# Kernel optimization log

Measured on AMD Instinct MI355X. Metric: run time of the kernel, lower is better.

## Reference

```python
import jax, jax.numpy as jnp
import numpy as np

EPS = 1e-6
TOPK = 5            # k = min(5, n_cluster)
SIGMA_HI = 1e4      # 10000 upper bound of binary search


def _pairwise_dist(z, mu, eps):
    # torch: sqrt(sum_d (z_id - mu_jd + eps)^2). Expanded algebraically to avoid the
    # (N, K, D) broadcast intermediate: (a-b+e)^2 = a^2 + b^2 + e^2 - 2ab + 2e(a-b).
    Dh = z.shape[1]
    z2 = jnp.sum(z * z, axis=1, keepdims=True)            # (N,1)
    m2 = jnp.sum(mu * mu, axis=1)[None, :]                # (1,K)
    cross = z @ mu.T                                      # (N,K)
    lin = 2.0 * eps * (jnp.sum(z, axis=1, keepdims=True) - jnp.sum(mu, axis=1)[None, :])
    d2 = z2 + m2 - 2.0 * cross + lin + Dh * (eps * eps)
    return jnp.sqrt(jnp.maximum(d2, 0.0))


def _calibrate_sigmas(rel_z, rel_u, rho_z, rho_u, k):
    # UMAP-style binary search. rel_z: (N,k) smallest dists per sample (ascending),
    # rel_u: (K,k) smallest dists per center. sigma values only ever flow from the
    # constant {0, SIGMA_HI} bounds, so this carries no gradient (matches torch).
    N = rel_z.shape[0]
    K = rel_u.shape[0]
    target = np.float32(np.log2(k) - 1.0)
    target1 = np.float32(np.log2(k))
    mid_z = jnp.concatenate([jnp.zeros((N, 1), jnp.float32), SIGMA_HI * jnp.ones((N, 1), jnp.float32)], axis=1)
    sigma_z = jnp.ones((N, 1), jnp.float32)
    mid_u = jnp.concatenate([jnp.zeros((K, 1), jnp.float32), SIGMA_HI * jnp.ones((K, 1), jnp.float32)], axis=1)
    sigma_u = jnp.ones((1, K), jnp.float32)
    rel_u_t = rel_u.T                                     # (k,K)

    def body(state, _):
        mid_u, sigma_u, mid_z, sigma_z = state
        current_u = jnp.sum(jnp.exp(-jax.nn.relu(rel_u_t - rho_u) / sigma_u), axis=0)   # (K,)
        idx_u = (current_u > target1).astype(jnp.int32)
        mid_u = mid_u.at[jnp.arange(K), idx_u].set(sigma_u[0])
        sigma_u = jnp.mean(mid_u, axis=1)[None, :]
        current_z = jnp.sum(jnp.exp(-jax.nn.relu(rel_z - rho_z) / sigma_z), axis=1)     # (N,)
        idx_z = (current_z > target).astype(jnp.int32)
        mid_z = mid_z.at[jnp.arange(N), idx_z].set(sigma_z[:, 0])
        sigma_z = jnp.mean(mid_z, axis=1)[:, None]
        return (mid_u, sigma_u, mid_z, sigma_z), None

    state, _ = jax.lax.scan(body, (mid_u, sigma_u, mid_z, sigma_z), None, length=k * 30)
    return state[3], state[1]  # sigma_z (N,1), sigma_u (1,K)


def compute_S(z, mu, epoch):
    sg = jax.lax.stop_gradient
    d_ = _pairwise_dist(z, mu, EPS)                       # (N,K)
    k = min(TOPK, mu.shape[0])
    rel_z = -jax.lax.top_k(-d_, k)[0]                     # (N,k) k smallest, ascending
    rel_u = -jax.lax.top_k(-d_.T, k)[0]                   # (K,k)
    rho_z = rel_z[:, :1]                                  # (N,1) nearest center per sample
    rho_u = rel_u[:, 0][None, :]                          # (1,K) nearest sample per center
    sigma_z, sigma_u = _calibrate_sigmas(sg(rel_z), sg(rel_u), sg(rho_z), sg(rho_u), k)
    rho_z = sg(rho_z)                                     # torch .detach()
    rho_u = sg(rho_u)
    W1 = jnp.exp(-jax.nn.relu(d_ - rho_z) / sigma_z)      # (N,K)
    W2 = jnp.exp(-jax.nn.relu(d_ - rho_u) / sigma_u)      # (N,K)
    S = W1 + W2 - W1 * W2
    S = S / jnp.sum(S, axis=1, keepdims=True)
    Dmat = (S * S) / jnp.sum(S, axis=0)                   # column-normalized sharpening
    Dmat = Dmat / jnp.sum(Dmat, axis=1, keepdims=True)
    return (W1, S, W1, Dmat)


def setup_inputs() -> dict:
    key = jax.random.key(0)
    kz, km = jax.random.split(key)
    z = jax.random.normal(kz, (65536, 256), dtype=jnp.float32)
    mu = jax.random.normal(km, (256, 256), dtype=jnp.float32)
    return {"z": z, "mu": mu, "epoch": 1}


def reference(z, mu, epoch):
    return compute_S(z, mu, epoch)
```

## Files before the change

### kernel.cpp

```cpp
#include <hip/hip_runtime.h>
#include <math.h>
#include <float.h>

#define KN 65536
#define KK 256
#define KD 256
#define KNK (65536LL * 256LL)
#define EPS_C 1e-6f
#define TARGET_Z 1.3219280948873622f
#define TARGET_U 2.3219280948873622f


__device__ __forceinline__ void ins5(float v, float& t0, float& t1, float& t2,
                                     float& t3, float& t4) {
    if (v < t4) {
        t4 = v; float tmp;
        if (t4 < t3) { tmp = t3; t3 = t4; t4 = tmp; }
        if (t3 < t2) { tmp = t2; t2 = t3; t3 = tmp; }
        if (t2 < t1) { tmp = t1; t1 = t2; t2 = tmp; }
        if (t1 < t0) { tmp = t0; t0 = t1; t1 = tmp; }
    }
}

__device__ __forceinline__ float bisect_sigma(float g1, float g2, float g3,
                                              float g4, float target) {
    float lo = 0.f, hi = 10000.f, sigma = 1.f;
    #pragma unroll 1
    for (int it = 0; it < 150; ++it) {
        float inv = 1.f / sigma;
        float s = 1.f + expf(-g1 * inv) + expf(-g2 * inv) +
                  expf(-g3 * inv) + expf(-g4 * inv);
        if (s > target) hi = sigma; else lo = sigma;
        sigma = 0.5f * (lo + hi);
    }
    return sigma;
}


__global__ __launch_bounds__(256) void row_stats(const float* __restrict__ x,
                                                 float* __restrict__ xs,
                                                 float* __restrict__ x2) {
    int wave = threadIdx.x >> 6, lane = threadIdx.x & 63;
    int row = blockIdx.x * 4 + wave;
    const float4* p = (const float4*)(x + (size_t)row * KD);
    float4 v = p[lane];
    float s = v.x + v.y + v.z + v.w;
    float q = v.x * v.x + v.y * v.y + v.z * v.z + v.w * v.w;
    #pragma unroll
    for (int off = 32; off > 0; off >>= 1) {
        s += __shfl_down(s, off, 64);
        q += __shfl_down(q, off, 64);
    }
    if (lane == 0) { xs[row] = s; x2[row] = q; }
}

__global__ __launch_bounds__(256) void dist_gemm(const float* __restrict__ z,
                                                 const float* __restrict__ mu,
                                                 const float* __restrict__ zs,
                                                 const float* __restrict__ z2,
                                                 const float* __restrict__ ms,
                                                 const float* __restrict__ m2,
                                                 float* __restrict__ dout) {
    __shared__ __align__(16) float As[16][132];
    __shared__ __align__(16) float Bs[16][132];
    int tid = threadIdx.x;
    int r0 = blockIdx.y * 128;
    int c0 = blockIdx.x * 128;
    int tx = tid & 15, ty = tid >> 4;
    float acc[8][8];
    #pragma unroll
    for (int i = 0; i < 8; ++i)
        #pragma unroll
        for (int j = 0; j < 8; ++j) acc[i][j] = 0.f;

    for (int kk = 0; kk < KD; kk += 16) {
        #pragma unroll
        for (int i = 0; i < 2; ++i) {
            int f = tid + 256 * i;
            int row = f >> 2, q = f & 3;
            float4 va = *(const float4*)(z + (size_t)(r0 + row) * KD + kk + 4 * q);
            As[4 * q + 0][row] = va.x; As[4 * q + 1][row] = va.y;
            As[4 * q + 2][row] = va.z; As[4 * q + 3][row] = va.w;
            float4 vb = *(const float4*)(mu + (size_t)(c0 + row) * KD + kk + 4 * q);
            Bs[4 * q + 0][row] = vb.x; Bs[4 * q + 1][row] = vb.y;
            Bs[4 * q + 2][row] = vb.z; Bs[4 * q + 3][row] = vb.w;
        }
        __syncthreads();
        #pragma unroll
        for (int k = 0; k < 16; ++k) {
            float4 a0 = *(const float4*)&As[k][ty * 8];
            float4 a1 = *(const float4*)&As[k][ty * 8 + 4];
            float4 b0 = *(const float4*)&Bs[k][tx * 8];
            float4 b1 = *(const float4*)&Bs[k][tx * 8 + 4];
            float a[8] = {a0.x, a0.y, a0.z, a0.w, a1.x, a1.y, a1.z, a1.w};
            float b[8] = {b0.x, b0.y, b0.z, b0.w, b1.x, b1.y, b1.z, b1.w};
            #pragma unroll
            for (int i = 0; i < 8; ++i)
                #pragma unroll
                for (int j = 0; j < 8; ++j) acc[i][j] += a[i] * b[j];
        }
        __syncthreads();
    }
    #pragma unroll
    for (int i = 0; i < 8; ++i) {
        int r = r0 + ty * 8 + i;
        float z2r = z2[r], zsr = zs[r];
        float out[8];
        #pragma unroll
        for (int j = 0; j < 8; ++j) {
            int c = c0 + tx * 8 + j;
            float d2 = z2r + m2[c] - 2.f * acc[i][j] +
                       2.f * EPS_C * (zsr - ms[c]) + (float)KD * EPS_C * EPS_C;
            out[j] = sqrtf(fmaxf(d2, 0.f));
        }
        float4* dst = (float4*)(dout + (size_t)r * KK + c0 + tx * 8);
        dst[0] = make_float4(out[0], out[1], out[2], out[3]);
        dst[1] = make_float4(out[4], out[5], out[6], out[7]);
    }
}

__global__ __launch_bounds__(256) void row_top5_sigma(const float* __restrict__ d,
                                                      float* __restrict__ rho_z,
                                                      float* __restrict__ isz) {
    int row = blockIdx.x * 256 + threadIdx.x;
    const float4* p = (const float4*)(d + (size_t)row * KK);
    float t0 = FLT_MAX, t1 = FLT_MAX, t2 = FLT_MAX, t3 = FLT_MAX, t4 = FLT_MAX;
    #pragma unroll 8
    for (int j = 0; j < KK / 4; ++j) {
        float4 v = p[j];
        ins5(v.x, t0, t1, t2, t3, t4); ins5(v.y, t0, t1, t2, t3, t4);
        ins5(v.z, t0, t1, t2, t3, t4); ins5(v.w, t0, t1, t2, t3, t4);
    }
    float sigma = bisect_sigma(t1 - t0, t2 - t0, t3 - t0, t4 - t0, TARGET_Z);
    rho_z[row] = t0;
    isz[row] = 1.f / sigma;
}

__global__ __launch_bounds__(256) void col_partial_top5(const float* __restrict__ d,
                                                        float* __restrict__ partials) {
    int b = blockIdx.x, t = threadIdx.x;
    size_t base = (size_t)b * 256 * KK + t;
    float t0 = FLT_MAX, t1 = FLT_MAX, t2 = FLT_MAX, t3 = FLT_MAX, t4 = FLT_MAX;
    #pragma unroll 8
    for (int r = 0; r < 256; ++r) ins5(d[base + (size_t)r * KK], t0, t1, t2, t3, t4);
    float* out = partials + ((size_t)t * 256 + b) * 5;
    out[0] = t0; out[1] = t1; out[2] = t2; out[3] = t3; out[4] = t4;
}

__global__ __launch_bounds__(64) void col_sigma(const float* __restrict__ partials,
                                                float* __restrict__ rho_u,
                                                float* __restrict__ isu) {
    int c = blockIdx.x * 64 + threadIdx.x;
    const float4* p = (const float4*)(partials + (size_t)c * 1280);
    float t0 = FLT_MAX, t1 = FLT_MAX, t2 = FLT_MAX, t3 = FLT_MAX, t4 = FLT_MAX;
    #pragma unroll 4
    for (int i = 0; i < 320; ++i) {
        float4 v = p[i];
        ins5(v.x, t0, t1, t2, t3, t4); ins5(v.y, t0, t1, t2, t3, t4);
        ins5(v.z, t0, t1, t2, t3, t4); ins5(v.w, t0, t1, t2, t3, t4);
    }
    float sigma = bisect_sigma(t1 - t0, t2 - t0, t3 - t0, t4 - t0, TARGET_U);
    rho_u[c] = t0;
    isu[c] = 1.f / sigma;
}

__global__ __launch_bounds__(256) void rowsum_su(const float* __restrict__ d,
                                                 const float* __restrict__ rho_z,
                                                 const float* __restrict__ isz,
                                                 const float* __restrict__ rho_u,
                                                 const float* __restrict__ isu,
                                                 float* __restrict__ irowsum) {
    int row = blockIdx.x * 256 + threadIdx.x;
    float rz = rho_z[row], sz = isz[row];
    const float4* p = (const float4*)(d + (size_t)row * KK);
    const float4* RU = (const float4*)rho_u;
    const float4* IU = (const float4*)isu;
    float sum = 0.f;
    #pragma unroll 4
    for (int j = 0; j < KK / 4; ++j) {
        float4 v = p[j], ru = RU[j], iu = IU[j];
        float w1, w2;
        w1 = expf(-fmaxf(v.x - rz, 0.f) * sz); w2 = expf(-fmaxf(v.x - ru.x, 0.f) * iu.x);
        sum += w1 + w2 - w1 * w2;
        w1 = expf(-fmaxf(v.y - rz, 0.f) * sz); w2 = expf(-fmaxf(v.y - ru.y, 0.f) * iu.y);
        sum += w1 + w2 - w1 * w2;
        w1 = expf(-fmaxf(v.z - rz, 0.f) * sz); w2 = expf(-fmaxf(v.z - ru.z, 0.f) * iu.z);
        sum += w1 + w2 - w1 * w2;
        w1 = expf(-fmaxf(v.w - rz, 0.f) * sz); w2 = expf(-fmaxf(v.w - ru.w, 0.f) * iu.w);
        sum += w1 + w2 - w1 * w2;
    }
    irowsum[row] = 1.f / sum;
}

__global__ __launch_bounds__(256) void w1_s_pass(const float* __restrict__ d,
                                                 const float* __restrict__ rho_z,
                                                 const float* __restrict__ isz,
                                                 const float* __restrict__ rho_u,
                                                 const float* __restrict__ isu,
                                                 const float* __restrict__ irowsum,
                                                 float* __restrict__ out0,
                                                 float* __restrict__ out1,
                                                 float* __restrict__ out2,
                                                 float* __restrict__ colsum) {
    int t = threadIdx.x;
    int r0 = blockIdx.x * 64;
    float ru = rho_u[t], iu = isu[t];
    float csum = 0.f;
    for (int r = 0; r < 64; ++r) {
        int row = r0 + r;
        size_t idx = (size_t)row * KK + t;
        float dv = d[idx];
        float rz = rho_z[row], sz = isz[row], ir = irowsum[row];
        float w1 = expf(-fmaxf(dv - rz, 0.f) * sz);
        float w2 = expf(-fmaxf(dv - ru, 0.f) * iu);
        float su = w1 + w2 - w1 * w2;
        float s = su * ir;
        out0[idx] = w1;
        out2[idx] = w1;
        out1[idx] = s;
        csum += s;
    }
    atomicAdd(&colsum[t], csum);
}

__global__ __launch_bounds__(256) void invert256(const float* __restrict__ colsum,
                                                 float* __restrict__ icol) {
    int t = threadIdx.x;
    icol[t] = 1.f / colsum[t];
}

__global__ __launch_bounds__(256) void rowsum_d(const float* __restrict__ S,
                                                const float* __restrict__ icol,
                                                float* __restrict__ irowD) {
    int row = blockIdx.x * 256 + threadIdx.x;
    const float4* p = (const float4*)(S + (size_t)row * KK);
    const float4* IC = (const float4*)icol;
    float sum = 0.f;
    #pragma unroll 4
    for (int j = 0; j < KK / 4; ++j) {
        float4 v = p[j], ic = IC[j];
        sum += v.x * v.x * ic.x + v.y * v.y * ic.y +
               v.z * v.z * ic.z + v.w * v.w * ic.w;
    }
    irowD[row] = 1.f / sum;
}

__global__ __launch_bounds__(256) void dmat_pass(const float* __restrict__ S,
                                                 const float* __restrict__ icol,
                                                 const float* __restrict__ irowD,
                                                 float* __restrict__ out3) {
    int t = threadIdx.x;
    int r0 = blockIdx.x * 64;
    float ic = icol[t];
    for (int r = 0; r < 64; ++r) {
        int row = r0 + r;
        size_t idx = (size_t)row * KK + t;
        float s = S[idx];
        out3[idx] = s * s * ic * irowD[row];
    }
}


extern "C" void kernel_launch(void* const* d_in, const int* in_sizes, int n_in,
                              void* d_out, int out_size, void* d_ws, size_t ws_size,
                              hipStream_t stream) {
    const float* z  = (const float*)d_in[0];
    const float* mu = (const float*)d_in[1];

    float* out = (float*)d_out;
    float* out0 = out;
    float* out1 = out + KNK;
    float* out2 = out + 2 * KNK;
    float* out3 = out + 3 * KNK;

    float* w = (float*)d_ws;
    float* zs       = w;
    float* z2       = w + KN;
    float* rho_z    = w + 2 * (size_t)KN;
    float* isz      = w + 3 * (size_t)KN;
    float* irowsum  = w + 4 * (size_t)KN;
    float* irowD    = w + 5 * (size_t)KN;
    float* ms       = w + 6 * (size_t)KN;
    float* m2       = ms + KK;
    float* rho_u    = m2 + KK;
    float* isu      = rho_u + KK;
    float* colsum   = isu + KK;
    float* icol     = colsum + KK;
    float* partials = icol + KK + 256;

    float* dmat = out3;

    hipMemsetAsync(colsum, 0, KK * sizeof(float), stream);

    row_stats<<<KN / 4, 256, 0, stream>>>(z, zs, z2);
    row_stats<<<KK / 4, 256, 0, stream>>>(mu, ms, m2);

    dist_gemm<<<dim3(KK / 128, KN / 128), 256, 0, stream>>>(z, mu, zs, z2, ms, m2, dmat);

    row_top5_sigma<<<KN / 256, 256, 0, stream>>>(dmat, rho_z, isz);

    col_partial_top5<<<KN / 256, 256, 0, stream>>>(dmat, partials);
    col_sigma<<<KK / 64, 64, 0, stream>>>(partials, rho_u, isu);

    rowsum_su<<<KN / 256, 256, 0, stream>>>(dmat, rho_z, isz, rho_u, isu, irowsum);

    w1_s_pass<<<KN / 64, 256, 0, stream>>>(dmat, rho_z, isz, rho_u, isu, irowsum,
                                           out0, out1, out2, colsum);

    invert256<<<1, 256, 0, stream>>>(colsum, icol);

    rowsum_d<<<KN / 256, 256, 0, stream>>>(out1, icol, irowD);

    dmat_pass<<<KN / 64, 256, 0, stream>>>(out1, icol, irowD, out3);
}
```

Baseline: 752.5 us.

## Fuse row top-5 and sigma into GEMM epilogue, fuse row-sum passes, coalesce column reductions

The distance GEMM now computes full 64x256 row tiles, so each block can extract the per-row top-5 with wave shuffles and run the sigma bisection in its epilogue. This removes the separate row top-5 kernel and its re-read of the distance matrix. The separate row-sum kernels for S and Dmat are folded into the element-wise passes by reducing across the 32 lanes that share a row. The column top-5 uses coalesced float4 loads plus a shared-memory merge, col_sigma uses one block per column with a shuffle merge, and bisection uses fast __expf. Trade-offs: more LDS use and register pressure in the GEMM, and slightly different exp precision.

```diff
diff --git a/kernel.cpp b/kernel.cpp
--- a/kernel.cpp
+++ b/kernel.cpp
@@ -9,6 +9,9 @@
 #define EPS_C 1e-6f
 #define TARGET_Z 1.3219280948873622f
 #define TARGET_U 2.3219280948873622f
+
+#define AS_LD 68
+#define BS_LD 260
 
 
 __device__ __forceinline__ void ins5(float v, float& t0, float& t1, float& t2,
@@ -28,8 +31,8 @@
     #pragma unroll 1
     for (int it = 0; it < 150; ++it) {
         float inv = 1.f / sigma;
-        float s = 1.f + expf(-g1 * inv) + expf(-g2 * inv) +
-                  expf(-g3 * inv) + expf(-g4 * inv);
+        float s = 1.f + __expf(-g1 * inv) + __expf(-g2 * inv) +
+                  __expf(-g3 * inv) + __expf(-g4 * inv);
         if (s > target) hi = sigma; else lo = sigma;
         sigma = 0.5f * (lo + hi);
     }
@@ -54,44 +57,51 @@
     if (lane == 0) { xs[row] = s; x2[row] = q; }
 }
 
-__global__ __launch_bounds__(256) void dist_gemm(const float* __restrict__ z,
-                                                 const float* __restrict__ mu,
-                                                 const float* __restrict__ zs,
-                                                 const float* __restrict__ z2,
-                                                 const float* __restrict__ ms,
-                                                 const float* __restrict__ m2,
-                                                 float* __restrict__ dout) {
-    __shared__ __align__(16) float As[16][132];
-    __shared__ __align__(16) float Bs[16][132];
+__global__ __launch_bounds__(256, 2) void dist_fused(
+    const float* __restrict__ z, const float* __restrict__ mu,
+    const float* __restrict__ zs, const float* __restrict__ z2,
+    const float* __restrict__ ms, const float* __restrict__ m2,
+    float* __restrict__ dout, float* __restrict__ rho_z,
+    float* __restrict__ isz) {
+    __shared__ __align__(16) float As[32 * AS_LD];
+    __shared__ __align__(16) float Bs[32 * BS_LD];
     int tid = threadIdx.x;
-    int r0 = blockIdx.y * 128;
-    int c0 = blockIdx.x * 128;
-    int tx = tid & 15, ty = tid >> 4;
+    int r0 = blockIdx.x * 64;
+    int tx = tid & 31, ty = tid >> 5;
     float acc[8][8];
     #pragma unroll
     for (int i = 0; i < 8; ++i)
         #pragma unroll
         for (int j = 0; j < 8; ++j) acc[i][j] = 0.f;
 
-    for (int kk = 0; kk < KD; kk += 16) {
+    for (int kk = 0; kk < KD; kk += 32) {
         #pragma unroll
         for (int i = 0; i < 2; ++i) {
             int f = tid + 256 * i;
-            int row = f >> 2, q = f & 3;
-            float4 va = *(const float4*)(z + (size_t)(r0 + row) * KD + kk + 4 * q);
-            As[4 * q + 0][row] = va.x; As[4 * q + 1][row] = va.y;
-            As[4 * q + 2][row] = va.z; As[4 * q + 3][row] = va.w;
-            float4 vb = *(const float4*)(mu + (size_t)(c0 + row) * KD + kk + 4 * q);
-            Bs[4 * q + 0][row] = vb.x; Bs[4 * q + 1][row] = vb.y;
-            Bs[4 * q + 2][row] = vb.z; Bs[4 * q + 3][row] = vb.w;
+            int row = f >> 3, q = f & 7;
+            float4 v = *(const float4*)(z + (size_t)(r0 + row) * KD + kk + 4 * q);
+            As[(4 * q + 0) * AS_LD + row] = v.x;
+            As[(4 * q + 1) * AS_LD + row] = v.y;
+            As[(4 * q + 2) * AS_LD + row] = v.z;
+            As[(4 * q + 3) * AS_LD + row] = v.w;
+        }
+        #pragma unroll
+        for (int i = 0; i < 8; ++i) {
+            int f = tid + 256 * i;
+            int col = f >> 3, q = f & 7;
+            float4 v = *(const float4*)(mu + (size_t)col * KD + kk + 4 * q);
+            Bs[(4 * q + 0) * BS_LD + col] = v.x;
+            Bs[(4 * q + 1) * BS_LD + col] = v.y;
+            Bs[(4 * q + 2) * BS_LD + col] = v.z;
+            Bs[(4 * q + 3) * BS_LD + col] = v.w;
         }
         __syncthreads();
         #pragma unroll
-        for (int k = 0; k < 16; ++k) {
-            float4 a0 = *(const float4*)&As[k][ty * 8];
-            float4 a1 = *(const float4*)&As[k][ty * 8 + 4];
-            float4 b0 = *(const float4*)&Bs[k][tx * 8];
-            float4 b1 = *(const float4*)&Bs[k][tx * 8 + 4];
+        for (int k = 0; k < 32; ++k) {
+            float4 a0 = *(const float4*)&As[k * AS_LD + ty * 8];
+            float4 a1 = *(const float4*)&As[k * AS_LD + ty * 8 + 4];
+            float4 b0 = *(const float4*)&Bs[k * BS_LD + tx * 4];
+            float4 b1 = *(const float4*)&Bs[k * BS_LD + 128 + tx * 4];
             float a[8] = {a0.x, a0.y, a0.z, a0.w, a1.x, a1.y, a1.z, a1.w};
             float b[8] = {b0.x, b0.y, b0.z, b0.w, b1.x, b1.y, b1.z, b1.w};
             #pragma unroll
@@ -101,162 +111,206 @@
         }
         __syncthreads();
     }
+
+    int c0 = 4 * tx, c1 = 128 + 4 * tx;
+    float4 m2a = *(const float4*)(m2 + c0);
+    float4 m2b = *(const float4*)(m2 + c1);
+    float4 msa = *(const float4*)(ms + c0);
+    float4 msb = *(const float4*)(ms + c1);
+    float m2v[8] = {m2a.x, m2a.y, m2a.z, m2a.w, m2b.x, m2b.y, m2b.z, m2b.w};
+    float msv[8] = {msa.x, msa.y, msa.z, msa.w, msb.x, msb.y, msb.z, msb.w};
+
+    float s0 = 0.f, s1 = 0.f, s2 = 0.f, s3 = 0.f, s4 = 0.f;
     #pragma unroll
     for (int i = 0; i < 8; ++i) {
         int r = r0 + ty * 8 + i;
         float z2r = z2[r], zsr = zs[r];
-        float out[8];
+        float dv[8];
         #pragma unroll
         for (int j = 0; j < 8; ++j) {
-            int c = c0 + tx * 8 + j;
-            float d2 = z2r + m2[c] - 2.f * acc[i][j] +
-                       2.f * EPS_C * (zsr - ms[c]) + (float)KD * EPS_C * EPS_C;
-            out[j] = sqrtf(fmaxf(d2, 0.f));
-        }
-        float4* dst = (float4*)(dout + (size_t)r * KK + c0 + tx * 8);
-        dst[0] = make_float4(out[0], out[1], out[2], out[3]);
-        dst[1] = make_float4(out[4], out[5], out[6], out[7]);
-    }
-}
-
-__global__ __launch_bounds__(256) void row_top5_sigma(const float* __restrict__ d,
-                                                      float* __restrict__ rho_z,
-                                                      float* __restrict__ isz) {
-    int row = blockIdx.x * 256 + threadIdx.x;
-    const float4* p = (const float4*)(d + (size_t)row * KK);
-    float t0 = FLT_MAX, t1 = FLT_MAX, t2 = FLT_MAX, t3 = FLT_MAX, t4 = FLT_MAX;
-    #pragma unroll 8
-    for (int j = 0; j < KK / 4; ++j) {
-        float4 v = p[j];
-        ins5(v.x, t0, t1, t2, t3, t4); ins5(v.y, t0, t1, t2, t3, t4);
-        ins5(v.z, t0, t1, t2, t3, t4); ins5(v.w, t0, t1, t2, t3, t4);
-    }
-    float sigma = bisect_sigma(t1 - t0, t2 - t0, t3 - t0, t4 - t0, TARGET_Z);
-    rho_z[row] = t0;
-    isz[row] = 1.f / sigma;
-}
-
-__global__ __launch_bounds__(256) void col_partial_top5(const float* __restrict__ d,
-                                                        float* __restrict__ partials) {
-    int b = blockIdx.x, t = threadIdx.x;
-    size_t base = (size_t)b * 256 * KK + t;
-    float t0 = FLT_MAX, t1 = FLT_MAX, t2 = FLT_MAX, t3 = FLT_MAX, t4 = FLT_MAX;
-    #pragma unroll 8
-    for (int r = 0; r < 256; ++r) ins5(d[base + (size_t)r * KK], t0, t1, t2, t3, t4);
-    float* out = partials + ((size_t)t * 256 + b) * 5;
-    out[0] = t0; out[1] = t1; out[2] = t2; out[3] = t3; out[4] = t4;
+            float d2 = z2r + m2v[j] - 2.f * acc[i][j] +
+                       2.f * EPS_C * (zsr - msv[j]) + (float)KD * EPS_C * EPS_C;
+            dv[j] = sqrtf(fmaxf(d2, 0.f));
+        }
+        *(float4*)(dout + (size_t)r * KK + c0) = make_float4(dv[0], dv[1], dv[2], dv[3]);
+        *(float4*)(dout + (size_t)r * KK + c1) = make_float4(dv[4], dv[5], dv[6], dv[7]);
+        float t0 = FLT_MAX, t1 = FLT_MAX, t2 = FLT_MAX, t3 = FLT_MAX, t4 = FLT_MAX;
+        #pragma unroll
+        for (int j = 0; j < 8; ++j) ins5(dv[j], t0, t1, t2, t3, t4);
+        #pragma unroll
+        for (int m = 1; m < 32; m <<= 1) {
+            float u0 = __shfl_xor(t0, m, 64), u1 = __shfl_xor(t1, m, 64);
+            float u2 = __shfl_xor(t2, m, 64), u3 = __shfl_xor(t3, m, 64);
+            float u4 = __shfl_xor(t4, m, 64);
+            ins5(u0, t0, t1, t2, t3, t4); ins5(u1, t0, t1, t2, t3, t4);
+            ins5(u2, t0, t1, t2, t3, t4); ins5(u3, t0, t1, t2, t3, t4);
+            ins5(u4, t0, t1, t2, t3, t4);
+        }
+        if (tx == i) { s0 = t0; s1 = t1; s2 = t2; s3 = t3; s4 = t4; }
+    }
+    if (tx < 8) {
+        int r = r0 + ty * 8 + tx;
+        float sigma = bisect_sigma(s1 - s0, s2 - s0, s3 - s0, s4 - s0, TARGET_Z);
+        rho_z[r] = s0;
+        isz[r] = 1.f / sigma;
+    }
+}
+
+__global__ __launch_bounds__(256) void col_partial(const float* __restrict__ d,
+                                                   float* __restrict__ partials) {
+    __shared__ float sm[4][64][20];
+    int tid = threadIdx.x;
+    int w = tid >> 6, l = tid & 63;
+    int rbase = blockIdx.x * 256 + w * 64;
+    float t[4][5];
+    #pragma unroll
+    for (int c = 0; c < 4; ++c)
+        #pragma unroll
+        for (int j = 0; j < 5; ++j) t[c][j] = FLT_MAX;
+    for (int r = 0; r < 64; ++r) {
+        float4 v = *(const float4*)(d + (size_t)(rbase + r) * KK + 4 * l);
+        ins5(v.x, t[0][0], t[0][1], t[0][2], t[0][3], t[0][4]);
+        ins5(v.y, t[1][0], t[1][1], t[1][2], t[1][3], t[1][4]);
+        ins5(v.z, t[2][0], t[2][1], t[2][2], t[2][3], t[2][4]);
+        ins5(v.w, t[3][0], t[3][1], t[3][2], t[3][3], t[3][4]);
+    }
+    #pragma unroll
+    for (int c = 0; c < 4; ++c)
+        #pragma unroll
+        for (int j = 0; j < 5; ++j) sm[w][l][c * 5 + j] = t[c][j];
+    __syncthreads();
+    if (tid < 64) {
+        #pragma unroll
+        for (int c = 0; c < 4; ++c) {
+            float p0 = sm[0][tid][c * 5 + 0], p1 = sm[0][tid][c * 5 + 1];
+            float p2 = sm[0][tid][c * 5 + 2], p3 = sm[0][tid][c * 5 + 3];
+            float p4 = sm[0][tid][c * 5 + 4];
+            #pragma unroll
+            for (int w2 = 1; w2 < 4; ++w2)
+                #pragma unroll
+                for (int j = 0; j < 5; ++j)
+                    ins5(sm[w2][tid][c * 5 + j], p0, p1, p2, p3, p4);
+            float* out = partials + ((size_t)(4 * tid + c) * 256 + blockIdx.x) * 5;
+            out[0] = p0; out[1] = p1; out[2] = p2; out[3] = p3; out[4] = p4;
+        }
+    }
 }
 
 __global__ __launch_bounds__(64) void col_sigma(const float* __restrict__ partials,
                                                 float* __restrict__ rho_u,
                                                 float* __restrict__ isu) {
-    int c = blockIdx.x * 64 + threadIdx.x;
-    const float4* p = (const float4*)(partials + (size_t)c * 1280);
+    int c = blockIdx.x, l = threadIdx.x;
+    const float* p = partials + (size_t)c * 1280 + l * 20;
     float t0 = FLT_MAX, t1 = FLT_MAX, t2 = FLT_MAX, t3 = FLT_MAX, t4 = FLT_MAX;
-    #pragma unroll 4
-    for (int i = 0; i < 320; ++i) {
-        float4 v = p[i];
+    #pragma unroll
+    for (int i = 0; i < 5; ++i) {
+        float4 v = *(const float4*)(p + 4 * i);
         ins5(v.x, t0, t1, t2, t3, t4); ins5(v.y, t0, t1, t2, t3, t4);
         ins5(v.z, t0, t1, t2, t3, t4); ins5(v.w, t0, t1, t2, t3, t4);
     }
-    float sigma = bisect_sigma(t1 - t0, t2 - t0, t3 - t0, t4 - t0, TARGET_U);
-    rho_u[c] = t0;
-    isu[c] = 1.f / sigma;
-}
-
-__global__ __launch_bounds__(256) void rowsum_su(const float* __restrict__ d,
-                                                 const float* __restrict__ rho_z,
-                                                 const float* __restrict__ isz,
-                                                 const float* __restrict__ rho_u,
-                                                 const float* __restrict__ isu,
-                                                 float* __restrict__ irowsum) {
-    int row = blockIdx.x * 256 + threadIdx.x;
-    float rz = rho_z[row], sz = isz[row];
-    const float4* p = (const float4*)(d + (size_t)row * KK);
-    const float4* RU = (const float4*)rho_u;
-    const float4* IU = (const float4*)isu;
-    float sum = 0.f;
-    #pragma unroll 4
-    for (int j = 0; j < KK / 4; ++j) {
-        float4 v = p[j], ru = RU[j], iu = IU[j];
-        float w1, w2;
-        w1 = expf(-fmaxf(v.x - rz, 0.f) * sz); w2 = expf(-fmaxf(v.x - ru.x, 0.f) * iu.x);
-        sum += w1 + w2 - w1 * w2;
-        w1 = expf(-fmaxf(v.y - rz, 0.f) * sz); w2 = expf(-fmaxf(v.y - ru.y, 0.f) * iu.y);
-        sum += w1 + w2 - w1 * w2;
-        w1 = expf(-fmaxf(v.z - rz, 0.f) * sz); w2 = expf(-fmaxf(v.z - ru.z, 0.f) * iu.z);
-        sum += w1 + w2 - w1 * w2;
-        w1 = expf(-fmaxf(v.w - rz, 0.f) * sz); w2 = expf(-fmaxf(v.w - ru.w, 0.f) * iu.w);
-        sum += w1 + w2 - w1 * w2;
-    }
-    irowsum[row] = 1.f / sum;
-}
-
-__global__ __launch_bounds__(256) void w1_s_pass(const float* __restrict__ d,
-                                                 const float* __restrict__ rho_z,
-                                                 const float* __restrict__ isz,
-                                                 const float* __restrict__ rho_u,
-                                                 const float* __restrict__ isu,
-                                                 const float* __restrict__ irowsum,
-                                                 float* __restrict__ out0,
-                                                 float* __restrict__ out1,
-                                                 float* __restrict__ out2,
-                                                 float* __restrict__ colsum) {
-    int t = threadIdx.x;
+    #pragma unroll
+    for (int m = 1; m < 64; m <<= 1) {
+        float u0 = __shfl_xor(t0, m, 64), u1 = __shfl_xor(t1, m, 64);
+        float u2 = __shfl_xor(t2, m, 64), u3 = __shfl_xor(t3, m, 64);
+        float u4 = __shfl_xor(t4, m, 64);
+        ins5(u0, t0, t1, t2, t3, t4); ins5(u1, t0, t1, t2, t3, t4);
+        ins5(u2, t0, t1, t2, t3, t4); ins5(u3, t0, t1, t2, t3, t4);
+        ins5(u4, t0, t1, t2, t3, t4);
+    }
+    if (l == 0) {
+        float sigma = bisect_sigma(t1 - t0, t2 - t0, t3 - t0, t4 - t0, TARGET_U);
+        rho_u[c] = t0;
+        isu[c] = 1.f / sigma;
+    }
+}
+
+__global__ __launch_bounds__(256) void su_pass(const float* __restrict__ d,
+                                               const float* __restrict__ rho_z,
+                                               const float* __restrict__ isz,
+                                               const float* __restrict__ rho_u,
+                                               const float* __restrict__ isu,
+                                               float* __restrict__ out0,
+                                               float* __restrict__ out1,
+                                               float* __restrict__ out2,
+                                               float* __restrict__ colsum) {
+    __shared__ float sm[8][256];
+    int tid = threadIdx.x, tx = tid & 31, ty = tid >> 5;
     int r0 = blockIdx.x * 64;
-    float ru = rho_u[t], iu = isu[t];
-    float csum = 0.f;
-    for (int r = 0; r < 64; ++r) {
-        int row = r0 + r;
-        size_t idx = (size_t)row * KK + t;
-        float dv = d[idx];
-        float rz = rho_z[row], sz = isz[row], ir = irowsum[row];
-        float w1 = expf(-fmaxf(dv - rz, 0.f) * sz);
-        float w2 = expf(-fmaxf(dv - ru, 0.f) * iu);
-        float su = w1 + w2 - w1 * w2;
-        float s = su * ir;
-        out0[idx] = w1;
-        out2[idx] = w1;
-        out1[idx] = s;
-        csum += s;
-    }
-    atomicAdd(&colsum[t], csum);
+    int cb = 8 * tx;
+    float4 rua = *(const float4*)(rho_u + cb);
+    float4 rub = *(const float4*)(rho_u + cb + 4);
+    float4 iua = *(const float4*)(isu + cb);
+    float4 iub = *(const float4*)(isu + cb + 4);
+    float ru[8] = {rua.x, rua.y, rua.z, rua.w, rub.x, rub.y, rub.z, rub.w};
+    float iu[8] = {iua.x, iua.y, iua.z, iua.w, iub.x, iub.y, iub.z, iub.w};
+    float cl[8] = {0.f, 0.f, 0.f, 0.f, 0.f, 0.f, 0.f, 0.f};
+    #pragma unroll 1
+    for (int i = 0; i < 8; ++i) {
+        int r = r0 + ty * 8 + i;
+        float rz = rho_z[r], sz = isz[r];
+        float4 d0 = *(const float4*)(d + (size_t)r * KK + cb);
+        float4 d1 = *(const float4*)(d + (size_t)r * KK + cb + 4);
+        float dvv[8] = {d0.x, d0.y, d0.z, d0.w, d1.x, d1.y, d1.z, d1.w};
+        float w1[8], su[8];
+        float rs = 0.f;
+        #pragma unroll
+        for (int j = 0; j < 8; ++j) {
+            w1[j] = __expf(-fmaxf(dvv[j] - rz, 0.f) * sz);
+            float w2 = __expf(-fmaxf(dvv[j] - ru[j], 0.f) * iu[j]);
+            su[j] = w1[j] + w2 - w1[j] * w2;
+            rs += su[j];
+        }
+        #pragma unroll
+        for (int m = 1; m < 32; m <<= 1) rs += __shfl_xor(rs, m, 64);
+        float ir = 1.f / rs;
+        *(float4*)(out0 + (size_t)r * KK + cb)     = make_float4(w1[0], w1[1], w1[2], w1[3]);
+        *(float4*)(out0 + (size_t)r * KK + cb + 4) = make_float4(w1[4], w1[5], w1[6], w1[7]);
+        *(float4*)(out2 + (size_t)r * KK + cb)     = make_float4(w1[0], w1[1], w1[2], w1[3]);
+        *(float4*)(out2 + (size_t)r * KK + cb + 4) = make_float4(w1[4], w1[5], w1[6], w1[7]);
+        float s[8];
+        #pragma unroll
+        for (int j = 0; j < 8; ++j) { s[j] = su[j] * ir; cl[j] += s[j]; }
+        *(float4*)(out1 + (size_t)r * KK + cb)     = make_float4(s[0], s[1], s[2], s[3]);
+        *(float4*)(out1 + (size_t)r * KK + cb + 4) = make_float4(s[4], s[5], s[6], s[7]);
+    }
+    #pragma unroll
+    for (int j = 0; j < 8; ++j) sm[ty][cb + j] = cl[j];
+    __syncthreads();
+    float a = 0.f;
+    #pragma unroll
+    for (int g = 0; g < 8; ++g) a += sm[g][tid];
+    atomicAdd(&colsum[tid], a);
 }
 
 __global__ __launch_bounds__(256) void invert256(const float* __restrict__ colsum,
                                                  float* __restrict__ icol) {
-    int t = threadIdx.x;
-    icol[t] = 1.f / colsum[t];
-}
-
-__global__ __launch_bounds__(256) void rowsum_d(const float* __restrict__ S,
-                                                const float* __restrict__ icol,
-                                                float* __restrict__ irowD) {
-    int row = blockIdx.x * 256 + threadIdx.x;
-    const float4* p = (const float4*)(S + (size_t)row * KK);
-    const float4* IC = (const float4*)icol;
-    float sum = 0.f;
-    #pragma unroll 4
-    for (int j = 0; j < KK / 4; ++j) {
-        float4 v = p[j], ic = IC[j];
-        sum += v.x * v.x * ic.x + v.y * v.y * ic.y +
-               v.z * v.z * ic.z + v.w * v.w * ic.w;
-    }
-    irowD[row] = 1.f / sum;
-}
-
-__global__ __launch_bounds__(256) void dmat_pass(const float* __restrict__ S,
-                                                 const float* __restrict__ icol,
-                                                 const float* __restrict__ irowD,
-                                                 float* __restrict__ out3) {
-    int t = threadIdx.x;
+    icol[threadIdx.x] = 1.f / colsum[threadIdx.x];
+}
+
+__global__ __launch_bounds__(256) void dmat_fused(const float* __restrict__ S,
+                                                  const float* __restrict__ icol,
+                                                  float* __restrict__ out3) {
+    int tid = threadIdx.x, tx = tid & 31, ty = tid >> 5;
     int r0 = blockIdx.x * 64;
-    float ic = icol[t];
-    for (int r = 0; r < 64; ++r) {
-        int row = r0 + r;
-        size_t idx = (size_t)row * KK + t;
-        float s = S[idx];
-        out3[idx] = s * s * ic * irowD[row];
+    int cb = 8 * tx;
+    float4 ic0 = *(const float4*)(icol + cb);
+    float4 ic1 = *(const float4*)(icol + cb + 4);
+    float ic[8] = {ic0.x, ic0.y, ic0.z, ic0.w, ic1.x, ic1.y, ic1.z, ic1.w};
+    #pragma unroll 1
+    for (int i = 0; i < 8; ++i) {
+        int r = r0 + ty * 8 + i;
+        float4 v0 = *(const float4*)(S + (size_t)r * KK + cb);
+        float4 v1 = *(const float4*)(S + (size_t)r * KK + cb + 4);
+        float sv[8] = {v0.x, v0.y, v0.z, v0.w, v1.x, v1.y, v1.z, v1.w};
+        float dp[8];
+        float rs = 0.f;
+        #pragma unroll
+        for (int j = 0; j < 8; ++j) { dp[j] = sv[j] * sv[j] * ic[j]; rs += dp[j]; }
+        #pragma unroll
+        for (int m = 1; m < 32; m <<= 1) rs += __shfl_xor(rs, m, 64);
+        float ir = 1.f / rs;
+        *(float4*)(out3 + (size_t)r * KK + cb)     = make_float4(dp[0] * ir, dp[1] * ir, dp[2] * ir, dp[3] * ir);
+        *(float4*)(out3 + (size_t)r * KK + cb + 4) = make_float4(dp[4] * ir, dp[5] * ir, dp[6] * ir, dp[7] * ir);
     }
 }
 
@@ -278,9 +332,7 @@
     float* z2       = w + KN;
     float* rho_z    = w + 2 * (size_t)KN;
     float* isz      = w + 3 * (size_t)KN;
-    float* irowsum  = w + 4 * (size_t)KN;
-    float* irowD    = w + 5 * (size_t)KN;
-    float* ms       = w + 6 * (size_t)KN;
+    float* ms       = w + 4 * (size_t)KN;
     float* m2       = ms + KK;
     float* rho_u    = m2 + KK;
     float* isu      = rho_u + KK;
@@ -295,21 +347,15 @@
     row_stats<<<KN / 4, 256, 0, stream>>>(z, zs, z2);
     row_stats<<<KK / 4, 256, 0, stream>>>(mu, ms, m2);
 
-    dist_gemm<<<dim3(KK / 128, KN / 128), 256, 0, stream>>>(z, mu, zs, z2, ms, m2, dmat);
-
-    row_top5_sigma<<<KN / 256, 256, 0, stream>>>(dmat, rho_z, isz);
-
-    col_partial_top5<<<KN / 256, 256, 0, stream>>>(dmat, partials);
-    col_sigma<<<KK / 64, 64, 0, stream>>>(partials, rho_u, isu);
-
-    rowsum_su<<<KN / 256, 256, 0, stream>>>(dmat, rho_z, isz, rho_u, isu, irowsum);
-
-    w1_s_pass<<<KN / 64, 256, 0, stream>>>(dmat, rho_z, isz, rho_u, isu, irowsum,
-                                           out0, out1, out2, colsum);
+    dist_fused<<<KN / 64, 256, 0, stream>>>(z, mu, zs, z2, ms, m2, dmat, rho_z, isz);
+
+    col_partial<<<KN / 256, 256, 0, stream>>>(dmat, partials);
+    col_sigma<<<KK, 64, 0, stream>>>(partials, rho_u, isu);
+
+    su_pass<<<KN / 64, 256, 0, stream>>>(dmat, rho_z, isz, rho_u, isu,
+                                         out0, out1, out2, colsum);
 
     invert256<<<1, 256, 0, stream>>>(colsum, icol);
 
-    rowsum_d<<<KN / 256, 256, 0, stream>>>(out1, icol, irowD);
-
-    dmat_pass<<<KN / 64, 256, 0, stream>>>(out1, icol, irowD, out3);
-}
+    dmat_fused<<<KN / 64, 256, 0, stream>>>(out1, icol, out3);
+}
```

New measurement: 613.4 us. 1.23x faster.
